# Optimization experiments

Measured on AMD Instinct MI355X. Metric: run time of the kernel, lower is better.

The kernel has to match this reference:

```python
import jax, jax.numpy as jnp
import numpy as np

N_NODES, D_NODE = 100000, 128
N_EDGES, D_EDGE = 1000000, 32
D_IN = 2 * D_NODE + D_EDGE  # 288
H1, H2, D_OUT = 128, 64, 1


def setup_inputs() -> dict:
    key = jax.random.key(0)
    ks = jax.random.split(key, 9)
    x = jax.random.normal(ks[0], (N_NODES, D_NODE), dtype=jnp.float32)
    edge_index = jax.random.randint(ks[1], (2, N_EDGES), 0, N_NODES, dtype=jnp.int64)
    edge_features = jax.random.normal(ks[2], (N_EDGES, D_EDGE), dtype=jnp.float32)
    def lin(kw, kb, fan_in, fan_out):
        bound = 1.0 / np.sqrt(fan_in)
        W = jax.random.uniform(kw, (fan_in, fan_out), minval=-bound, maxval=bound, dtype=jnp.float32)
        b = jax.random.uniform(kb, (fan_out,), minval=-bound, maxval=bound, dtype=jnp.float32)
        return W, b
    W1, b1 = lin(ks[3], ks[4], D_IN, H1)
    W2, b2 = lin(ks[5], ks[6], H1, H2)
    W3, b3 = lin(ks[7], ks[8], H2, D_OUT)
    return {"x": x, "edge_index": edge_index, "edge_features": edge_features,
            "W1": W1, "b1": b1, "W2": W2, "b2": b2, "W3": W3, "b3": b3}


def reference(x, edge_index, edge_features, W1, b1, W2, b2, W3, b3):
    origin, destination = edge_index[0], edge_index[1]
    # [E, 2*D_NODE + D_EDGE]
    z = jnp.concatenate([x[origin], x[destination], edge_features], axis=1)
    z = jax.nn.leaky_relu(z @ W1 + b1)  # negative_slope=0.01, matches torch default
    z = jax.nn.leaky_relu(z @ W2 + b2)
    z = z @ W3 + b3
    return z.reshape(-1)
```

## Files before the change

### kernel.cpp

```cpp
#include <hip/hip_runtime.h>

#define N_NODES 100000
#define N_EDGES 1000000

typedef __attribute__((ext_vector_type(8))) short bf16x8;
typedef __attribute__((ext_vector_type(4))) float f32x4;
typedef __attribute__((ext_vector_type(4))) unsigned u32x4;

static __device__ __forceinline__ short f2bf(float f) {
    unsigned u = __float_as_uint(f);
    u = (u + 0x7fffu + ((u >> 16) & 1u)) >> 16;
    return (short)u;
}
static __device__ __forceinline__ float bf2f(unsigned short s) {
    return __uint_as_float(((unsigned)s) << 16);
}
static __device__ __forceinline__ float lrelu(float x) {
    return fmaxf(x, 0.01f * x);
}
static __device__ __forceinline__ unsigned cvtpk(float lo, float hi) {
    unsigned r;
    asm("v_cvt_pk_bf16_f32 %0, %1, %2" : "=v"(r) : "v"(lo), "v"(hi));
    return r;
}
static __device__ __forceinline__ f32x4 ldnt_f4(const float* p) {
    return __builtin_nontemporal_load((const f32x4*)p);
}
static __device__ __forceinline__ int ldnt_i(const int* p) {
    return __builtin_nontemporal_load(p);
}

__global__ __launch_bounds__(256) void precompute_mfma(
    const float* __restrict__ x, const float* __restrict__ W1,
    const float* __restrict__ b1, unsigned short* __restrict__ Pb,
    unsigned short* __restrict__ Qb)
{
    const int t    = threadIdx.x;
    const int lane = t & 63;
    const int w    = t >> 6;
    const int q    = lane >> 4;
    const int n15  = lane & 15;
    const int chb  = 64 * w;

    bf16x8 afrag[4][4];
    #pragma unroll
    for (int mtl = 0; mtl < 4; ++mtl) {
        const int ch = chb + 16 * mtl + n15;
        const float* wcol = (ch < 128) ? (W1 + ch) : (W1 + 128 * 128 + (ch - 128));
        #pragma unroll
        for (int ks = 0; ks < 4; ++ks)
            #pragma unroll
            for (int j = 0; j < 8; ++j)
                afrag[mtl][ks][j] = f2bf(wcol[(size_t)(32 * ks + 8 * q + j) * 128]);
    }
    float b1r[16];
    #pragma unroll
    for (int mtl = 0; mtl < 4; ++mtl)
        #pragma unroll
        for (int r = 0; r < 4; ++r) {
            const int ch = chb + 16 * mtl + 4 * q + r;
            b1r[mtl * 4 + r] = (ch < 128) ? b1[ch] : 0.0f;
        }

    unsigned short* tbase = (w < 2) ? Pb : Qb;
    const int mtb = 4 * (w & 1);

    for (int tile = blockIdx.x; tile < N_NODES / 16; tile += gridDim.x) {
        const int n0 = tile * 16;
        const float* xrow = x + (size_t)(n0 + n15) * 128;

        bf16x8 bfr[4];
        #pragma unroll
        for (int ks = 0; ks < 4; ++ks) {
            f32x4 xa = ldnt_f4(xrow + 32 * ks + 8 * q);
            f32x4 xb = ldnt_f4(xrow + 32 * ks + 8 * q + 4);
            u32x4 bu;
            bu[0] = cvtpk(xa[0], xa[1]);
            bu[1] = cvtpk(xa[2], xa[3]);
            bu[2] = cvtpk(xb[0], xb[1]);
            bu[3] = cvtpk(xb[2], xb[3]);
            bfr[ks] = __builtin_bit_cast(bf16x8, bu);
        }
        #pragma unroll
        for (int mtl = 0; mtl < 4; ++mtl) {
            f32x4 acc = {0.f, 0.f, 0.f, 0.f};
            #pragma unroll
            for (int ks = 0; ks < 4; ++ks)
                acc = __builtin_amdgcn_mfma_f32_16x16x32_bf16(afrag[mtl][ks], bfr[ks], acc, 0, 0, 0);
            unsigned* dst = (unsigned*)(tbase + (size_t)(n0 + n15) * 128 + q * 32 + (mtb + mtl) * 4);
            dst[0] = cvtpk(acc[0] + b1r[mtl * 4 + 0], acc[1] + b1r[mtl * 4 + 1]);
            dst[1] = cvtpk(acc[2] + b1r[mtl * 4 + 2], acc[3] + b1r[mtl * 4 + 3]);
        }
    }
}

__global__ __launch_bounds__(256, 3) void edge_mfma(
    const int* __restrict__ ei, const float* __restrict__ ef,
    const float* __restrict__ W1, const float* __restrict__ W2,
    const float* __restrict__ b2, const float* __restrict__ W3,
    const float* __restrict__ b3, const unsigned short* __restrict__ Pb,
    const unsigned short* __restrict__ Qb, float* __restrict__ out)
{
    __shared__ unsigned short w2s[16 * 64 * 8];
    __shared__ unsigned short a1s[8 * 64 * 8];
    const int t    = threadIdx.x;
    const int lane = t & 63;
    const int w    = t >> 6;
    const int q    = lane >> 4;
    const int n15  = lane & 15;

    #pragma unroll
    for (int i = 0; i < 2; ++i) {
        const int mt = 2 * w + i;
        bf16x8 f;
        #pragma unroll
        for (int j = 0; j < 8; ++j)
            f[j] = f2bf(W1[(size_t)(256 + 8 * q + j) * 128 + 16 * mt + n15]);
        *(bf16x8*)&a1s[(mt * 64 + lane) * 8] = f;
    }

    {
        const int mt2 = w;
        #pragma unroll
        for (int ks = 0; ks < 4; ++ks) {
            bf16x8 f;
            #pragma unroll
            for (int j = 0; j < 8; ++j) {
                const int ch = 32 * ks + ((j < 4) ? (4 * q + j) : (16 + 4 * q + (j - 4)));
                f[j] = f2bf(W2[(size_t)ch * 64 + 16 * mt2 + n15]);
            }
            *(bf16x8*)&w2s[(((mt2 << 2) | ks) * 64 + lane) * 8] = f;
        }
    }

    unsigned b2w3[16];
    #pragma unroll
    for (int mt2 = 0; mt2 < 4; ++mt2)
        #pragma unroll
        for (int r = 0; r < 4; ++r) {
            const int ch = 16 * mt2 + 4 * q + r;
            b2w3[mt2 * 4 + r] = (unsigned)(unsigned short)f2bf(b2[ch])
                              | ((unsigned)(unsigned short)f2bf(W3[ch]) << 16);
        }
    const float b3v = b3[0];

    __syncthreads();

    const int nTiles  = N_EDGES / 16;
    const int wid     = blockIdx.x * 4 + w;
    const int wstride = gridDim.x * 4;
    if (wid >= nTiles) return;

    int tile0 = wid;
    int tile1 = tile0 + wstride;
    bool have1 = tile1 < nTiles;

    int oi0, di0; f32x4 ea0, eb0;
    {
        const int e0 = tile0 * 16;
        oi0 = ldnt_i(&ei[e0 + n15]);
        di0 = ldnt_i(&ei[N_EDGES + e0 + n15]);
        ea0 = ldnt_f4(ef + (size_t)(e0 + n15) * 32 + 8 * q);
        eb0 = ldnt_f4(ef + (size_t)(e0 + n15) * 32 + 8 * q + 4);
    }
    int oi1 = 0, di1 = 0; f32x4 ea1 = ea0, eb1 = eb0;
    if (have1) {
        const int e1 = tile1 * 16;
        oi1 = ldnt_i(&ei[e1 + n15]);
        di1 = ldnt_i(&ei[N_EDGES + e1 + n15]);
        ea1 = ldnt_f4(ef + (size_t)(e1 + n15) * 32 + 8 * q);
        eb1 = ldnt_f4(ef + (size_t)(e1 + n15) * 32 + 8 * q + 4);
    }
    bf16x8 pvb[4], qvb[4];
    {
        const unsigned short* prow = Pb + (size_t)oi0 * 128 + q * 32;
        const unsigned short* qrow = Qb + (size_t)di0 * 128 + q * 32;
        #pragma unroll
        for (int c = 0; c < 4; ++c) {
            pvb[c] = *(const bf16x8*)(prow + 8 * c);
            qvb[c] = *(const bf16x8*)(qrow + 8 * c);
        }
    }

    while (true) {
        u32x4 befu;
        befu[0] = cvtpk(ea0[0], ea0[1]);
        befu[1] = cvtpk(ea0[2], ea0[3]);
        befu[2] = cvtpk(eb0[0], eb0[1]);
        befu[3] = cvtpk(eb0[2], eb0[3]);
        const bf16x8 bef = __builtin_bit_cast(bf16x8, befu);

        const int  tile2 = tile1 + wstride;
        const bool have2 = have1 && (tile2 < nTiles);
        int oi2 = oi1, di2 = di1; f32x4 ea2 = ea1, eb2 = eb1;
        if (have2) {
            const int e2 = tile2 * 16;
            oi2 = ldnt_i(&ei[e2 + n15]);
            di2 = ldnt_i(&ei[N_EDGES + e2 + n15]);
            ea2 = ldnt_f4(ef + (size_t)(e2 + n15) * 32 + 8 * q);
            eb2 = ldnt_f4(ef + (size_t)(e2 + n15) * 32 + 8 * q + 4);
        }

        u32x4 hfu[4];
        #pragma unroll
        for (int mt = 0; mt < 8; ++mt) {
            const bf16x8 a1f = *(const bf16x8*)&a1s[(mt * 64 + lane) * 8];
            f32x4 z = {0.f, 0.f, 0.f, 0.f};
            f32x4 h = __builtin_amdgcn_mfma_f32_16x16x32_bf16(a1f, bef, z, 0, 0, 0);
            const int c = mt >> 1, off = (mt & 1) * 4;
            float v0 = lrelu(h[0] + bf2f((unsigned short)pvb[c][off + 0]) + bf2f((unsigned short)qvb[c][off + 0]));
            float v1 = lrelu(h[1] + bf2f((unsigned short)pvb[c][off + 1]) + bf2f((unsigned short)qvb[c][off + 1]));
            float v2 = lrelu(h[2] + bf2f((unsigned short)pvb[c][off + 2]) + bf2f((unsigned short)qvb[c][off + 2]));
            float v3 = lrelu(h[3] + bf2f((unsigned short)pvb[c][off + 3]) + bf2f((unsigned short)qvb[c][off + 3]));
            hfu[mt >> 1][(mt & 1) * 2 + 0] = cvtpk(v0, v1);
            hfu[mt >> 1][(mt & 1) * 2 + 1] = cvtpk(v2, v3);
        }

        if (have1) {
            const unsigned short* prow = Pb + (size_t)oi1 * 128 + q * 32;
            const unsigned short* qrow = Qb + (size_t)di1 * 128 + q * 32;
            #pragma unroll
            for (int c = 0; c < 4; ++c) {
                pvb[c] = *(const bf16x8*)(prow + 8 * c);
                qvb[c] = *(const bf16x8*)(qrow + 8 * c);
            }
        }

        f32x4 acc2[4] = {{0.f,0.f,0.f,0.f},{0.f,0.f,0.f,0.f},{0.f,0.f,0.f,0.f},{0.f,0.f,0.f,0.f}};
        #pragma unroll
        for (int ks = 0; ks < 4; ++ks) {
            const bf16x8 hfrag = __builtin_bit_cast(bf16x8, hfu[ks]);
            #pragma unroll
            for (int mt2 = 0; mt2 < 4; ++mt2) {
                const bf16x8 a2f = *(const bf16x8*)&w2s[(((mt2 << 2) | ks) * 64 + lane) * 8];
                acc2[mt2] = __builtin_amdgcn_mfma_f32_16x16x32_bf16(a2f, hfrag, acc2[mt2], 0, 0, 0);
            }
        }

        float s = 0.0f;
        #pragma unroll
        for (int mt2 = 0; mt2 < 4; ++mt2)
            #pragma unroll
            for (int r = 0; r < 4; ++r) {
                const unsigned u = b2w3[mt2 * 4 + r];
                float v = acc2[mt2][r] + bf2f((unsigned short)(u & 0xffffu));
                v = lrelu(v);
                s += v * __uint_as_float(u & 0xffff0000u);
            }
        s += __shfl_xor(s, 16);
        s += __shfl_xor(s, 32);
        if (q == 0) __builtin_nontemporal_store(s + b3v, &out[tile0 * 16 + n15]);

        if (!have1) break;
        tile0 = tile1; tile1 = tile2; have1 = have2;
        oi1 = oi2; di1 = di2;
        ea0 = ea1; eb0 = eb1; ea1 = ea2; eb1 = eb2;
    }
}

extern "C" void kernel_launch(void* const* d_in, const int* in_sizes, int n_in,
                              void* d_out, int out_size, void* d_ws, size_t ws_size,
                              hipStream_t stream) {
    const float* x   = (const float*)d_in[0];
    const int*   ei  = (const int*)d_in[1];
    const float* ef  = (const float*)d_in[2];
    const float* W1  = (const float*)d_in[3];
    const float* b1  = (const float*)d_in[4];
    const float* W2  = (const float*)d_in[5];
    const float* b2  = (const float*)d_in[6];
    const float* W3  = (const float*)d_in[7];
    const float* b3  = (const float*)d_in[8];
    float*       out = (float*)d_out;

    unsigned short* Pb = (unsigned short*)d_ws;
    unsigned short* Qb = Pb + (size_t)N_NODES * 128;

    precompute_mfma<<<512, 256, 0, stream>>>(x, W1, b1, Pb, Qb);
    edge_mfma<<<1536, 256, 0, stream>>>(ei, ef, W1, W2, b2, W3, b3, Pb, Qb, out);
}
```

Measured before the change: 340.5 us.

## Bucket-sort edges by origin node before edge MLP for gather locality

Adds a counting sort (histogram, scan, atomic scatter) that groups edges by origin node into buckets of 16 and packs origin, destination and edge id into a 64-bit key. The edge kernel then walks contiguous runs of sorted tiles per wave instead of a grid-strided order, gathers edge features through the stored edge id, and scatters results to out[eid]. The aim is better cache reuse of the Pb rows, at the cost of three extra kernel launches, atomics, an extra pass over the edge indices, and scattered edge-feature reads and output writes.

```diff
diff --git a/kernel.cpp b/kernel.cpp
--- a/kernel.cpp
+++ b/kernel.cpp
@@ -2,6 +2,9 @@
 
 #define N_NODES 100000
 #define N_EDGES 1000000
+#define SHIFT   4
+#define NBUCK   6250
+#define TPW     11
 
 typedef __attribute__((ext_vector_type(8))) short bf16x8;
 typedef __attribute__((ext_vector_type(4))) float f32x4;
@@ -26,8 +29,63 @@
 static __device__ __forceinline__ f32x4 ldnt_f4(const float* p) {
     return __builtin_nontemporal_load((const f32x4*)p);
 }
-static __device__ __forceinline__ int ldnt_i(const int* p) {
+static __device__ __forceinline__ unsigned long long ldnt_u64(const unsigned long long* p) {
     return __builtin_nontemporal_load(p);
+}
+
+__global__ __launch_bounds__(256) void sort_hist(
+    const int* __restrict__ ei, unsigned* __restrict__ gh)
+{
+    __shared__ unsigned lh[NBUCK];
+    const int t = threadIdx.x;
+    for (int i = t; i < NBUCK; i += 256) lh[i] = 0;
+    __syncthreads();
+    for (int e = blockIdx.x * 256 + t; e < N_EDGES; e += gridDim.x * 256)
+        atomicAdd(&lh[((unsigned)ei[e]) >> SHIFT], 1u);
+    __syncthreads();
+    for (int i = t; i < NBUCK; i += 256)
+        if (lh[i]) atomicAdd(&gh[i], lh[i]);
+}
+
+__global__ __launch_bounds__(256) void sort_scan(
+    const unsigned* __restrict__ gh, unsigned* __restrict__ cursor)
+{
+    __shared__ unsigned lh[NBUCK];
+    __shared__ unsigned sums[256];
+    const int t = threadIdx.x;
+    unsigned run = 0;
+    #pragma unroll
+    for (int j = 0; j < 25; ++j) {
+        const int idx = t * 25 + j;
+        if (idx < NBUCK) { lh[idx] = run; run += gh[idx]; }
+    }
+    sums[t] = run;
+    __syncthreads();
+    if (t == 0) {
+        unsigned acc = 0;
+        for (int i = 0; i < 256; ++i) { unsigned v = sums[i]; sums[i] = acc; acc += v; }
+    }
+    __syncthreads();
+    const unsigned base = sums[t];
+    #pragma unroll
+    for (int j = 0; j < 25; ++j) {
+        const int idx = t * 25 + j;
+        if (idx < NBUCK) cursor[idx] = lh[idx] + base;
+    }
+}
+
+__global__ __launch_bounds__(256) void sort_scatter(
+    const int* __restrict__ ei, unsigned* __restrict__ cursor,
+    unsigned long long* __restrict__ so)
+{
+    for (int e = blockIdx.x * 256 + threadIdx.x; e < N_EDGES; e += gridDim.x * 256) {
+        const unsigned oi = (unsigned)ei[e];
+        const unsigned di = (unsigned)ei[N_EDGES + e];
+        const unsigned pos = atomicAdd(&cursor[oi >> SHIFT], 1u);
+        so[pos] = (unsigned long long)oi
+                | ((unsigned long long)di << 20)
+                | ((unsigned long long)e  << 40);
+    }
 }
 
 __global__ __launch_bounds__(256) void precompute_mfma(
@@ -95,7 +153,7 @@
 }
 
 __global__ __launch_bounds__(256, 3) void edge_mfma(
-    const int* __restrict__ ei, const float* __restrict__ ef,
+    const unsigned long long* __restrict__ so, const float* __restrict__ ef,
     const float* __restrict__ W1, const float* __restrict__ W2,
     const float* __restrict__ b2, const float* __restrict__ W3,
     const float* __restrict__ b3, const unsigned short* __restrict__ Pb,
@@ -118,7 +176,6 @@
             f[j] = f2bf(W1[(size_t)(256 + 8 * q + j) * 128 + 16 * mt + n15]);
         *(bf16x8*)&a1s[(mt * 64 + lane) * 8] = f;
     }
-
     {
         const int mt2 = w;
         #pragma unroll
@@ -132,7 +189,6 @@
             *(bf16x8*)&w2s[(((mt2 << 2) | ks) * 64 + lane) * 8] = f;
         }
     }
-
     unsigned b2w3[16];
     #pragma unroll
     for (int mt2 = 0; mt2 < 4; ++mt2)
@@ -146,30 +202,28 @@
 
     __syncthreads();
 
-    const int nTiles  = N_EDGES / 16;
-    const int wid     = blockIdx.x * 4 + w;
-    const int wstride = gridDim.x * 4;
-    if (wid >= nTiles) return;
-
-    int tile0 = wid;
-    int tile1 = tile0 + wstride;
-    bool have1 = tile1 < nTiles;
-
-    int oi0, di0; f32x4 ea0, eb0;
+    const int nTiles = N_EDGES / 16;
+    const int wv     = blockIdx.x * 4 + w;
+    const int base   = wv * TPW;
+    if (base >= nTiles) return;
+    const int tileEnd = min(base + TPW, nTiles);
+
+    int tile0 = base, tile1 = base + 1;
+    bool have1 = tile1 < tileEnd;
+
+    int oi0, di0, eid0; f32x4 ea0, eb0;
     {
-        const int e0 = tile0 * 16;
-        oi0 = ldnt_i(&ei[e0 + n15]);
-        di0 = ldnt_i(&ei[N_EDGES + e0 + n15]);
-        ea0 = ldnt_f4(ef + (size_t)(e0 + n15) * 32 + 8 * q);
-        eb0 = ldnt_f4(ef + (size_t)(e0 + n15) * 32 + 8 * q + 4);
-    }
-    int oi1 = 0, di1 = 0; f32x4 ea1 = ea0, eb1 = eb0;
+        const unsigned long long s0 = ldnt_u64(&so[(size_t)tile0 * 16 + n15]);
+        oi0 = (int)(s0 & 0xFFFFFu); di0 = (int)((s0 >> 20) & 0xFFFFFu); eid0 = (int)(s0 >> 40);
+        ea0 = ldnt_f4(ef + (size_t)eid0 * 32 + 8 * q);
+        eb0 = ldnt_f4(ef + (size_t)eid0 * 32 + 8 * q + 4);
+    }
+    int oi1 = oi0, di1 = di0, eid1 = eid0; f32x4 ea1 = ea0, eb1 = eb0;
     if (have1) {
-        const int e1 = tile1 * 16;
-        oi1 = ldnt_i(&ei[e1 + n15]);
-        di1 = ldnt_i(&ei[N_EDGES + e1 + n15]);
-        ea1 = ldnt_f4(ef + (size_t)(e1 + n15) * 32 + 8 * q);
-        eb1 = ldnt_f4(ef + (size_t)(e1 + n15) * 32 + 8 * q + 4);
+        const unsigned long long s1 = ldnt_u64(&so[(size_t)tile1 * 16 + n15]);
+        oi1 = (int)(s1 & 0xFFFFFu); di1 = (int)((s1 >> 20) & 0xFFFFFu); eid1 = (int)(s1 >> 40);
+        ea1 = ldnt_f4(ef + (size_t)eid1 * 32 + 8 * q);
+        eb1 = ldnt_f4(ef + (size_t)eid1 * 32 + 8 * q + 4);
     }
     bf16x8 pvb[4], qvb[4];
     {
@@ -190,15 +244,14 @@
         befu[3] = cvtpk(eb0[2], eb0[3]);
         const bf16x8 bef = __builtin_bit_cast(bf16x8, befu);
 
-        const int  tile2 = tile1 + wstride;
-        const bool have2 = have1 && (tile2 < nTiles);
-        int oi2 = oi1, di2 = di1; f32x4 ea2 = ea1, eb2 = eb1;
+        const int  tile2 = tile1 + 1;
+        const bool have2 = have1 && (tile2 < tileEnd);
+        int oi2 = oi1, di2 = di1, eid2 = eid1; f32x4 ea2 = ea1, eb2 = eb1;
         if (have2) {
-            const int e2 = tile2 * 16;
-            oi2 = ldnt_i(&ei[e2 + n15]);
-            di2 = ldnt_i(&ei[N_EDGES + e2 + n15]);
-            ea2 = ldnt_f4(ef + (size_t)(e2 + n15) * 32 + 8 * q);
-            eb2 = ldnt_f4(ef + (size_t)(e2 + n15) * 32 + 8 * q + 4);
+            const unsigned long long s2 = ldnt_u64(&so[(size_t)tile2 * 16 + n15]);
+            oi2 = (int)(s2 & 0xFFFFFu); di2 = (int)((s2 >> 20) & 0xFFFFFu); eid2 = (int)(s2 >> 40);
+            ea2 = ldnt_f4(ef + (size_t)eid2 * 32 + 8 * q);
+            eb2 = ldnt_f4(ef + (size_t)eid2 * 32 + 8 * q + 4);
         }
 
         u32x4 hfu[4];
@@ -249,11 +302,12 @@
             }
         s += __shfl_xor(s, 16);
         s += __shfl_xor(s, 32);
-        if (q == 0) __builtin_nontemporal_store(s + b3v, &out[tile0 * 16 + n15]);
+        if (q == 0) __builtin_nontemporal_store(s + b3v, &out[eid0]);
 
         if (!have1) break;
         tile0 = tile1; tile1 = tile2; have1 = have2;
         oi1 = oi2; di1 = di2;
+        eid0 = eid1; eid1 = eid2;
         ea0 = ea1; eb0 = eb1; ea1 = ea2; eb1 = eb2;
     }
 }
@@ -274,7 +328,14 @@
 
     unsigned short* Pb = (unsigned short*)d_ws;
     unsigned short* Qb = Pb + (size_t)N_NODES * 128;
-
+    unsigned long long* so = (unsigned long long*)(Qb + (size_t)N_NODES * 128);
+    unsigned* gh     = (unsigned*)(so + (size_t)N_EDGES);
+    unsigned* cursor = gh + NBUCK;
+
+    hipMemsetAsync(gh, 0, NBUCK * sizeof(unsigned), stream);
+    sort_hist   <<<256, 256, 0, stream>>>(ei, gh);
+    sort_scan   <<<1,   256, 0, stream>>>(gh, cursor);
+    sort_scatter<<<1024,256, 0, stream>>>(ei, cursor, so);
     precompute_mfma<<<512, 256, 0, stream>>>(x, W1, b1, Pb, Qb);
-    edge_mfma<<<1536, 256, 0, stream>>>(ei, ef, W1, W2, b2, W3, b3, Pb, Qb, out);
-}
+    edge_mfma<<<1536, 256, 0, stream>>>(so, ef, W1, W2, b2, W3, b3, Pb, Qb, out);
+}
```

Result: slower. 473.8 us (+39.1%).
